# Performance work log

Measured on AMD Instinct MI355X. Metric: run time of the kernel, lower is better.

## Reference

```python
import jax, jax.numpy as jnp
import numpy as np

N = 100000      # nodes
E = 1600000     # edges
IN, H, OUT = 128, 128, 64
FUSION_W = 0.5


def setup_inputs() -> dict:
    key = jax.random.key(0)
    ks = jax.random.split(key, 10)
    x = jax.random.normal(ks[0], (N, IN), dtype=jnp.float32)
    edge_index = jax.random.randint(ks[1], (2, E), 0, N, dtype=jnp.int32)

    def lin(k, fi, fo):
        return jax.random.normal(k, (fi, fo), dtype=jnp.float32) / np.float32(np.sqrt(fi))

    return {
        "x": x,
        "edge_index": edge_index,
        "gnn_W1": lin(ks[2], IN, H),  "gnn_b1": jnp.zeros((H,), jnp.float32),
        "gnn_W2": lin(ks[3], H, OUT), "gnn_b2": jnp.zeros((OUT,), jnp.float32),
        "mlp_W1": lin(ks[4], IN, H),  "mlp_b1": jnp.zeros((H,), jnp.float32),
        "mlp_W2": lin(ks[5], H, OUT), "mlp_b2": jnp.zeros((OUT,), jnp.float32),
    }


def _gcn_conv(x, W, b, src, dst, deg_inv_sqrt, deg_inv):
    # GCNConv: x' = D^{-1/2} (A + I) D^{-1/2} (x W) + b, deg counts self-loops
    h = x @ W                                     # [N, F_out]
    norm = deg_inv_sqrt[src] * deg_inv_sqrt[dst]  # [E]
    agg = jax.ops.segment_sum(h[src] * norm[:, None], dst, num_segments=N)
    # self-loop contribution has norm 1/deg
    return agg + h * deg_inv[:, None] + b


def reference(x, edge_index, gnn_W1, gnn_b1, gnn_W2, gnn_b2,
              mlp_W1, mlp_b1, mlp_W2, mlp_b2):
    src, dst = edge_index[0], edge_index[1]
    # in-degree including self-loops (PyG GCNConv default add_self_loops=True)
    deg = 1.0 + jax.ops.segment_sum(jnp.ones((E,), jnp.float32), dst, num_segments=N)
    deg_inv_sqrt = jax.lax.rsqrt(deg)
    deg_inv = 1.0 / deg

    # GNN branch (dropout is identity in eval mode)
    h = jax.nn.relu(_gcn_conv(x, gnn_W1, gnn_b1, src, dst, deg_inv_sqrt, deg_inv))
    z_gnn = _gcn_conv(h, gnn_W2, gnn_b2, src, dst, deg_inv_sqrt, deg_inv)

    # MLP branch
    z_mlp = jax.nn.relu(x @ mlp_W1 + mlp_b1) @ mlp_W2 + mlp_b2

    return FUSION_W * z_gnn + (1.0 - FUSION_W) * z_mlp
```

## Files before the change

kernel.cpp:

```cpp
#include <hip/hip_runtime.h>
#include <hip/hip_fp16.h>

static constexpr int IN_F = 128;
static constexpr int FCAP = 6144;

typedef _Float16 half8 __attribute__((ext_vector_type(8)));
typedef _Float16 half4 __attribute__((ext_vector_type(4)));
typedef float f32x4 __attribute__((ext_vector_type(4)));
typedef float f32x2 __attribute__((ext_vector_type(2)));

__device__ inline void acc_fp8x8(uint2 u, f32x2* a) {
    a[0] += __builtin_amdgcn_cvt_pk_f32_fp8(u.x, false);
    a[1] += __builtin_amdgcn_cvt_pk_f32_fp8(u.x, true);
    a[2] += __builtin_amdgcn_cvt_pk_f32_fp8(u.y, false);
    a[3] += __builtin_amdgcn_cvt_pk_f32_fp8(u.y, true);
}
__device__ inline void acc_fp8x4(unsigned u, f32x2* a) {
    a[0] += __builtin_amdgcn_cvt_pk_f32_fp8(u, false);
    a[1] += __builtin_amdgcn_cvt_pk_f32_fp8(u, true);
}
__device__ inline void fp8x8_to_f32(uint2 u, float* f) {
    f32x2 a0 = __builtin_amdgcn_cvt_pk_f32_fp8(u.x, false);
    f32x2 a1 = __builtin_amdgcn_cvt_pk_f32_fp8(u.x, true);
    f32x2 a2 = __builtin_amdgcn_cvt_pk_f32_fp8(u.y, false);
    f32x2 a3 = __builtin_amdgcn_cvt_pk_f32_fp8(u.y, true);
    f[0] = a0[0]; f[1] = a0[1]; f[2] = a1[0]; f[3] = a1[1];
    f[4] = a2[0]; f[5] = a2[1]; f[6] = a3[0]; f[7] = a3[1];
}
__device__ inline void fp8x4_to_f32(unsigned u, float* f) {
    f32x2 a0 = __builtin_amdgcn_cvt_pk_f32_fp8(u, false);
    f32x2 a1 = __builtin_amdgcn_cvt_pk_f32_fp8(u, true);
    f[0] = a0[0]; f[1] = a0[1]; f[2] = a1[0]; f[3] = a1[1];
}
__device__ inline unsigned char f32_to_fp8(float v) {
    return (unsigned char)__builtin_amdgcn_cvt_pk_fp8_f32(v, v, 0, false);
}


__global__ __launch_bounds__(1024) void kb_count(const int* __restrict__ dst,
                                                 int* __restrict__ bcount, int E) {
    __shared__ int cnt[16][512];
    const int tid = threadIdx.x;
    const int wv  = tid >> 6;
    for (int i = tid; i < 16 * 512; i += 1024) (&cnt[0][0])[i] = 0;
    __syncthreads();
#pragma unroll
    for (int q = 0; q < 8; ++q) {
        int i = blockIdx.x * 8192 + q * 1024 + tid;
        if (i < E) atomicAdd(&cnt[wv][dst[i] >> 8], 1);
    }
    __syncthreads();
    if (tid < 512) {
        int run = 0;
#pragma unroll
        for (int w = 0; w < 16; ++w) run += cnt[w][tid];
        if (run > 0) atomicAdd(&bcount[tid], run);
    }
}

__global__ __launch_bounds__(512) void k_scanb(const int* __restrict__ bcount,
                                               int* __restrict__ bbase,
                                               int* __restrict__ bcursor, int NB) {
    __shared__ int s[512];
    const int tid = threadIdx.x;
    int v = (tid < NB) ? bcount[tid] : 0;
    s[tid] = v;
    __syncthreads();
    int inc = v;
#pragma unroll
    for (int off = 1; off < 512; off <<= 1) {
        int add = (tid >= off) ? s[tid - off] : 0;
        __syncthreads();
        s[tid] = inc = inc + add;
        __syncthreads();
    }
    if (tid < NB) { bbase[tid] = inc - v; bcursor[tid] = inc - v; }
    if (tid == NB - 1) bbase[NB] = inc;
}

__global__ __launch_bounds__(1024) void kb_move(const int* __restrict__ src,
                                                const int* __restrict__ dst,
                                                int* __restrict__ bcursor,
                                                unsigned* __restrict__ recs, int E) {
    __shared__ int cnt[16][512];
    __shared__ int gbase[512];
    const int tid = threadIdx.x;
    const int wv  = tid >> 6;
    for (int i = tid; i < 16 * 512; i += 1024) (&cnt[0][0])[i] = 0;
    __syncthreads();

    int bq[8];
    unsigned rq[8];
#pragma unroll
    for (int q = 0; q < 8; ++q) {
        int i = blockIdx.x * 8192 + q * 1024 + tid;
        if (i < E) {
            int d = dst[i];
            int s = src[i];
            bq[q] = d >> 8;
            rq[q] = (unsigned)(((d & 255) << 17) | s);
            atomicAdd(&cnt[wv][bq[q]], 1);
        } else {
            bq[q] = -1;
            rq[q] = 0u;
        }
    }
    __syncthreads();
    if (tid < 512) {
        int run = 0;
#pragma unroll
        for (int w = 0; w < 16; ++w) {
            int t = cnt[w][tid];
            cnt[w][tid] = run;
            run += t;
        }
        gbase[tid] = (run > 0) ? atomicAdd(&bcursor[tid], run) : 0;
    }
    __syncthreads();
#pragma unroll
    for (int q = 0; q < 8; ++q) {
        if (bq[q] >= 0) {
            int p = gbase[bq[q]] + atomicAdd(&cnt[wv][bq[q]], 1);
            recs[p] = rq[q];
        }
    }
}

__global__ __launch_bounds__(512) void kb_fill_lds(const unsigned* __restrict__ recs,
                                                   const int* __restrict__ bbase,
                                                   int* __restrict__ row_ptr,
                                                   float* __restrict__ dis,
                                                   int* __restrict__ csr, int n) {
    __shared__ int hist[256];
    __shared__ int sc[256];
    __shared__ int base[257];
    __shared__ int cur[256];
    __shared__ int stage[FCAP];
    const int tid   = threadIdx.x;
    const int b     = blockIdx.x;
    const int s     = bbase[b], e = bbase[b + 1];
    const int nbase = b << 8;

    if (tid < 256) hist[tid] = 0;
    __syncthreads();
    for (int i = s + tid; i < e; i += 512)
        atomicAdd(&hist[recs[i] >> 17], 1);
    __syncthreads();

    const int v = (tid < 256) ? hist[tid] : 0;
    if (tid < 256) sc[tid] = v;
    __syncthreads();
    int inc = v;
#pragma unroll
    for (int off = 1; off < 256; off <<= 1) {
        int add = (tid >= off && tid < 256) ? sc[tid - off] : 0;
        __syncthreads();
        if (tid < 256) sc[tid] = inc = inc + add;
        __syncthreads();
    }
    if (tid < 256) {
        const int excl = inc - v;
        base[tid] = excl;
        if (tid == 255) base[256] = inc;
        cur[tid] = 0;

        const int idx = nbase + tid;
        if (idx < n) {
            row_ptr[idx] = s + excl;
            dis[idx] = rsqrtf(1.0f + (float)v);
        }
        if (idx == n) row_ptr[n] = s + excl;
        if (tid == 255 && nbase + 256 == n) row_ptr[n] = s + inc;
    }
    __syncthreads();

    for (int i = s + tid; i < e; i += 512) {
        unsigned r = recs[i];
        int dl = (int)(r >> 17);
        int slot = base[dl] + atomicAdd(&cur[dl], 1);
        int sr = (int)(r & 0x1FFFFu);
        if (slot < FCAP) stage[slot] = sr;
        else csr[s + slot] = sr;
    }
    __syncthreads();

    const int total = e - s;
    const int lim = total < FCAP ? total : FCAP;
    for (int i = tid; i < lim; i += 512)
        csr[s + i] = stage[i];
}

__global__ __launch_bounds__(256) void k_prep_w(const float* __restrict__ gW1,
                                                const float* __restrict__ mW1,
                                                const float* __restrict__ mW2,
                                                const float* __restrict__ gW2,
                                                _Float16* __restrict__ tg1,
                                                _Float16* __restrict__ tm1,
                                                _Float16* __restrict__ tm2,
                                                _Float16* __restrict__ tg2) {
    int i = blockIdx.x * 256 + threadIdx.x;
    if (i < 16384)      { int j = i;         int f = j >> 7, k = j & 127; tg1[j] = (_Float16)gW1[k * 128 + f]; }
    else if (i < 32768) { int j = i - 16384; int f = j >> 7, k = j & 127; tm1[j] = (_Float16)mW1[k * 128 + f]; }
    else if (i < 40960) { int j = i - 32768; int f = j >> 7, k = j & 127; tm2[j] = (_Float16)mW2[k * 64 + f]; }
    else if (i < 49152) { int j = i - 40960; int f = j >> 7, k = j & 127; tg2[j] = (_Float16)gW2[k * 64 + f]; }
}

__global__ __launch_bounds__(256) void k_dual_mfma(const float* __restrict__ x,
                                                   const _Float16* __restrict__ tg1,
                                                   const _Float16* __restrict__ tm1,
                                                   const _Float16* __restrict__ tm2,
                                                   const float* __restrict__ b1,
                                                   const float* __restrict__ b2,
                                                   const float* __restrict__ dis,
                                                   unsigned char* __restrict__ h1,
                                                   _Float16* __restrict__ z, int nrows) {
    __shared__ _Float16 As[64 * 128];
    __shared__ _Float16 Ws[128 * 128];
    _Float16* Ms = As;
    const int tid  = threadIdx.x;
    const int row0 = blockIdx.x * 64;

#pragma unroll
    for (int p = 0; p < 4; ++p) {
        int sid = p * 256 + tid;
        int r = sid >> 4, s = sid & 15;
        int gr = row0 + r;
        uint4 v = make_uint4(0, 0, 0, 0);
        if (gr < nrows) {
            const float4 f0 = *reinterpret_cast<const float4*>(x + (size_t)gr * 128 + s * 8);
            const float4 f1 = *reinterpret_cast<const float4*>(x + (size_t)gr * 128 + s * 8 + 4);
            _Float16 t[8] = {(_Float16)f0.x, (_Float16)f0.y, (_Float16)f0.z, (_Float16)f0.w,
                             (_Float16)f1.x, (_Float16)f1.y, (_Float16)f1.z, (_Float16)f1.w};
            v = *reinterpret_cast<uint4*>(t);
        }
        *reinterpret_cast<uint4*>(&As[r * 128 + ((s ^ (r & 7)) * 8)]) = v;
    }
#pragma unroll
    for (int p = 0; p < 8; ++p) {
        int sid = p * 256 + tid;
        int r = sid >> 4, s = sid & 15;
        uint4 v = *reinterpret_cast<const uint4*>(tg1 + (size_t)r * 128 + s * 8);
        *reinterpret_cast<uint4*>(&Ws[r * 128 + ((s ^ (r & 7)) * 8)]) = v;
    }
    __syncthreads();

    const int lane = tid & 63;
    const int wv   = tid >> 6;
    const int mrow = wv * 16 + (lane & 15);
    const int kg   = lane >> 4;
    const int grow = row0 + wv * 16 + kg * 4;

    half8 a[4];
#pragma unroll
    for (int kk = 0; kk < 4; ++kk)
        a[kk] = *reinterpret_cast<const half8*>(&As[mrow * 128 + (((kk * 4 + kg) ^ (mrow & 7)) * 8)]);

    float dvals[4];
#pragma unroll
    for (int j = 0; j < 4; ++j)
        dvals[j] = (grow + j < nrows) ? dis[grow + j] : 0.f;

#pragma unroll
    for (int ct = 0; ct < 8; ++ct) {
        const int ncol = ct * 16 + (lane & 15);
        f32x4 acc = {0.f, 0.f, 0.f, 0.f};
#pragma unroll
        for (int kk = 0; kk < 4; ++kk) {
            half8 b = *reinterpret_cast<const half8*>(&Ws[ncol * 128 + (((kk * 4 + kg) ^ (ncol & 7)) * 8)]);
            acc = __builtin_amdgcn_mfma_f32_16x16x32_f16(a[kk], b, acc, 0, 0, 0);
        }
#pragma unroll
        for (int j = 0; j < 4; ++j)
            if (grow + j < nrows)
                h1[(size_t)(grow + j) * 128 + ncol] = f32_to_fp8(acc[j] * dvals[j]);
    }
    __syncthreads();

#pragma unroll
    for (int p = 0; p < 8; ++p) {
        int sid = p * 256 + tid;
        int r = sid >> 4, s = sid & 15;
        uint4 v = *reinterpret_cast<const uint4*>(tm1 + (size_t)r * 128 + s * 8);
        *reinterpret_cast<uint4*>(&Ws[r * 128 + ((s ^ (r & 7)) * 8)]) = v;
    }
    __syncthreads();

#pragma unroll
    for (int ct = 0; ct < 8; ++ct) {
        const int ncol = ct * 16 + (lane & 15);
        f32x4 acc = {0.f, 0.f, 0.f, 0.f};
#pragma unroll
        for (int kk = 0; kk < 4; ++kk) {
            half8 b = *reinterpret_cast<const half8*>(&Ws[ncol * 128 + (((kk * 4 + kg) ^ (ncol & 7)) * 8)]);
            acc = __builtin_amdgcn_mfma_f32_16x16x32_f16(a[kk], b, acc, 0, 0, 0);
        }
        const float bias = b1[ncol];
#pragma unroll
        for (int j = 0; j < 4; ++j) {
            int r = wv * 16 + kg * 4 + j;
            float v = fmaxf((float)acc[j] + bias, 0.f);
            Ms[r * 128 + (((ncol >> 3) ^ (r & 7)) * 8) + (ncol & 7)] = (_Float16)v;
        }
    }
    __syncthreads();

#pragma unroll
    for (int p = 0; p < 4; ++p) {
        int sid = p * 256 + tid;
        int r = sid >> 4, s = sid & 15;
        uint4 v = *reinterpret_cast<const uint4*>(tm2 + (size_t)r * 128 + s * 8);
        *reinterpret_cast<uint4*>(&Ws[r * 128 + ((s ^ (r & 7)) * 8)]) = v;
    }
    __syncthreads();

    half8 am[4];
#pragma unroll
    for (int kk = 0; kk < 4; ++kk)
        am[kk] = *reinterpret_cast<const half8*>(&Ms[mrow * 128 + (((kk * 4 + kg) ^ (mrow & 7)) * 8)]);

#pragma unroll
    for (int ct = 0; ct < 4; ++ct) {
        const int ncol = ct * 16 + (lane & 15);
        f32x4 acc = {0.f, 0.f, 0.f, 0.f};
#pragma unroll
        for (int kk = 0; kk < 4; ++kk) {
            half8 b = *reinterpret_cast<const half8*>(&Ws[ncol * 128 + (((kk * 4 + kg) ^ (ncol & 7)) * 8)]);
            acc = __builtin_amdgcn_mfma_f32_16x16x32_f16(am[kk], b, acc, 0, 0, 0);
        }
        const float bias = b2[ncol];
#pragma unroll
        for (int j = 0; j < 4; ++j)
            if (grow + j < nrows)
                z[(size_t)(grow + j) * 64 + ncol] = (_Float16)((float)acc[j] + bias);
    }
}

__global__ __launch_bounds__(256) void k_mm64(const _Float16* __restrict__ A,
                                              const _Float16* __restrict__ Wt,
                                              const float* __restrict__ dis,
                                              unsigned char* __restrict__ C, int nrows) {
    __shared__ _Float16 As[64 * 128];
    __shared__ _Float16 Ws[64 * 128];
    const int tid  = threadIdx.x;
    const int row0 = blockIdx.x * 64;

#pragma unroll
    for (int p = 0; p < 4; ++p) {
        int sid = p * 256 + tid;
        int r = sid >> 4, s = sid & 15;
        int gr = row0 + r;
        uint4 v = make_uint4(0, 0, 0, 0);
        if (gr < nrows) v = *reinterpret_cast<const uint4*>(A + (size_t)gr * 128 + s * 8);
        *reinterpret_cast<uint4*>(&As[r * 128 + ((s ^ (r & 7)) * 8)]) = v;
    }
#pragma unroll
    for (int p = 0; p < 4; ++p) {
        int sid = p * 256 + tid;
        int r = sid >> 4, s = sid & 15;
        uint4 v = *reinterpret_cast<const uint4*>(Wt + (size_t)r * 128 + s * 8);
        *reinterpret_cast<uint4*>(&Ws[r * 128 + ((s ^ (r & 7)) * 8)]) = v;
    }
    __syncthreads();

    const int lane = tid & 63;
    const int wv   = tid >> 6;
    const int mrow = wv * 16 + (lane & 15);
    const int kg   = lane >> 4;
    const int grow = row0 + wv * 16 + kg * 4;

    half8 a[4];
#pragma unroll
    for (int kk = 0; kk < 4; ++kk)
        a[kk] = *reinterpret_cast<const half8*>(&As[mrow * 128 + (((kk * 4 + kg) ^ (mrow & 7)) * 8)]);

    float dvals[4];
#pragma unroll
    for (int j = 0; j < 4; ++j)
        dvals[j] = (grow + j < nrows) ? dis[grow + j] : 0.f;

#pragma unroll
    for (int ct = 0; ct < 4; ++ct) {
        const int ncol = ct * 16 + (lane & 15);
        f32x4 acc = {0.f, 0.f, 0.f, 0.f};
#pragma unroll
        for (int kk = 0; kk < 4; ++kk) {
            half8 b = *reinterpret_cast<const half8*>(&Ws[ncol * 128 + (((kk * 4 + kg) ^ (ncol & 7)) * 8)]);
            acc = __builtin_amdgcn_mfma_f32_16x16x32_f16(a[kk], b, acc, 0, 0, 0);
        }
#pragma unroll
        for (int j = 0; j < 4; ++j)
            if (grow + j < nrows)
                C[(size_t)(grow + j) * 64 + ncol] = f32_to_fp8(acc[j] * dvals[j]);
    }
}

__global__ __launch_bounds__(256) void k_agg1(const int* __restrict__ rp,
                                              const int* __restrict__ csr,
                                              const float* __restrict__ dis,
                                              const unsigned char* __restrict__ h1,
                                              const float* __restrict__ b,
                                              _Float16* __restrict__ out, int n) {
    const int tid  = threadIdx.x;
    const int node = blockIdx.x * 4 + (tid >> 6);
    if (node >= n) return;
    const int lane = tid & 63;
    const int g    = lane >> 4;
    const int c0   = (lane & 15) * 8;
    const int start = rp[node], end = rp[node + 1];

    f32x2 acc[4] = {{0.f, 0.f}, {0.f, 0.f}, {0.f, 0.f}, {0.f, 0.f}};

    int j = start + g;
    for (; j + 12 < end; j += 16) {
        int s0 = csr[j];
        int s1 = csr[j + 4];
        int s2 = csr[j + 8];
        int s3 = csr[j + 12];
        uint2 u0 = *reinterpret_cast<const uint2*>(h1 + (size_t)s0 * 128 + c0);
        uint2 u1 = *reinterpret_cast<const uint2*>(h1 + (size_t)s1 * 128 + c0);
        uint2 u2 = *reinterpret_cast<const uint2*>(h1 + (size_t)s2 * 128 + c0);
        uint2 u3 = *reinterpret_cast<const uint2*>(h1 + (size_t)s3 * 128 + c0);
        acc_fp8x8(u0, acc);
        acc_fp8x8(u1, acc);
        acc_fp8x8(u2, acc);
        acc_fp8x8(u3, acc);
    }
    for (; j < end; j += 4) {
        int s0 = csr[j];
        uint2 u0 = *reinterpret_cast<const uint2*>(h1 + (size_t)s0 * 128 + c0);
        acc_fp8x8(u0, acc);
    }

    float av[8] = {acc[0][0], acc[0][1], acc[1][0], acc[1][1],
                   acc[2][0], acc[2][1], acc[3][0], acc[3][1]};
#pragma unroll
    for (int k = 0; k < 8; ++k) {
        av[k] += __shfl_xor(av[k], 16);
        av[k] += __shfl_xor(av[k], 32);
    }

    if (g == 0) {
        const float dd = dis[node];
        uint2 un = *reinterpret_cast<const uint2*>(h1 + (size_t)node * 128 + c0);
        float fn[8];
        fp8x8_to_f32(un, fn);
        const float4 bv0 = *reinterpret_cast<const float4*>(b + c0);
        const float4 bv1 = *reinterpret_cast<const float4*>(b + c0 + 4);
        const float bb[8] = {bv0.x, bv0.y, bv0.z, bv0.w, bv1.x, bv1.y, bv1.z, bv1.w};
        half8 o;
#pragma unroll
        for (int k = 0; k < 8; ++k)
            o[k] = (_Float16)fmaxf(dd * (av[k] + fn[k]) + bb[k], 0.f);
        *reinterpret_cast<half8*>(out + (size_t)node * 128 + c0) = o;
    }
}

__global__ __launch_bounds__(256) void k_agg2(const int* __restrict__ rp,
                                              const int* __restrict__ csr,
                                              const float* __restrict__ dis,
                                              const unsigned char* __restrict__ h2,
                                              const float* __restrict__ b,
                                              const _Float16* __restrict__ zmlp,
                                              float* __restrict__ out, int n) {
    const int tid  = threadIdx.x;
    const int node = blockIdx.x * 4 + (tid >> 6);
    if (node >= n) return;
    const int lane = tid & 63;
    const int g    = lane >> 4;
    const int c0   = (lane & 15) * 4;
    const int start = rp[node], end = rp[node + 1];

    f32x2 acc[2] = {{0.f, 0.f}, {0.f, 0.f}};

    int j = start + g;
    for (; j + 12 < end; j += 16) {
        int s0 = csr[j];
        int s1 = csr[j + 4];
        int s2 = csr[j + 8];
        int s3 = csr[j + 12];
        unsigned u0 = *reinterpret_cast<const unsigned*>(h2 + (size_t)s0 * 64 + c0);
        unsigned u1 = *reinterpret_cast<const unsigned*>(h2 + (size_t)s1 * 64 + c0);
        unsigned u2 = *reinterpret_cast<const unsigned*>(h2 + (size_t)s2 * 64 + c0);
        unsigned u3 = *reinterpret_cast<const unsigned*>(h2 + (size_t)s3 * 64 + c0);
        acc_fp8x4(u0, acc);
        acc_fp8x4(u1, acc);
        acc_fp8x4(u2, acc);
        acc_fp8x4(u3, acc);
    }
    for (; j < end; j += 4) {
        int s0 = csr[j];
        unsigned u0 = *reinterpret_cast<const unsigned*>(h2 + (size_t)s0 * 64 + c0);
        acc_fp8x4(u0, acc);
    }

    float av[4] = {acc[0][0], acc[0][1], acc[1][0], acc[1][1]};
#pragma unroll
    for (int k = 0; k < 4; ++k) {
        av[k] += __shfl_xor(av[k], 16);
        av[k] += __shfl_xor(av[k], 32);
    }

    if (g == 0) {
        const float dd = dis[node];
        unsigned un = *reinterpret_cast<const unsigned*>(h2 + (size_t)node * 64 + c0);
        float fn[4];
        fp8x4_to_f32(un, fn);
        half4 zm = *reinterpret_cast<const half4*>(zmlp + (size_t)node * 64 + c0);
        const float4 bv = *reinterpret_cast<const float4*>(b + c0);
        const float bb[4] = {bv.x, bv.y, bv.z, bv.w};
        float4 o;
        float* op = &o.x;
#pragma unroll
        for (int k = 0; k < 4; ++k)
            op[k] = 0.5f * ((dd * (av[k] + fn[k]) + bb[k]) + (float)zm[k]);
        *reinterpret_cast<float4*>(out + (size_t)node * 64 + c0) = o;
    }
}

extern "C" void kernel_launch(void* const* d_in, const int* in_sizes, int n_in,
                              void* d_out, int out_size, void* d_ws, size_t ws_size,
                              hipStream_t stream) {
    const float* x      = (const float*)d_in[0];
    const int* edge_idx = (const int*)d_in[1];
    const float* gnn_W1 = (const float*)d_in[2];
    const float* gnn_b1 = (const float*)d_in[3];
    const float* gnn_W2 = (const float*)d_in[4];
    const float* gnn_b2 = (const float*)d_in[5];
    const float* mlp_W1 = (const float*)d_in[6];
    const float* mlp_b1 = (const float*)d_in[7];
    const float* mlp_W2 = (const float*)d_in[8];
    const float* mlp_b2 = (const float*)d_in[9];
    float* out = (float*)d_out;

    const int N = in_sizes[0] / IN_F;
    const int E = in_sizes[1] / 2;
    const int* src = edge_idx;
    const int* dst = edge_idx + E;

    const int NB = (N + 255) >> 8;

    char* wp = (char*)d_ws;
    int* row_ptr   = (int*)wp;            wp += ((size_t)N + 4) * sizeof(int);
    int* bbase     = (int*)wp;            wp += 516 * sizeof(int);
    int* bcursor   = (int*)wp;            wp += 512 * sizeof(int);
    int* bcount    = (int*)wp;            wp += 512 * sizeof(int);
    int* csr       = (int*)wp;            wp += (size_t)E * sizeof(int);
    unsigned* recs = (unsigned*)wp;       wp += (size_t)E * sizeof(unsigned);
    float* dis     = (float*)wp;          wp += (size_t)N * sizeof(float);
    _Float16* tg1  = (_Float16*)wp;       wp += 16384 * sizeof(_Float16);
    _Float16* tm1  = (_Float16*)wp;       wp += 16384 * sizeof(_Float16);
    _Float16* tm2  = (_Float16*)wp;       wp += 8192 * sizeof(_Float16);
    _Float16* tg2  = (_Float16*)wp;       wp += 8192 * sizeof(_Float16);
    unsigned char* h1 = (unsigned char*)wp;  wp += (size_t)N * 128;
    _Float16* hmid = (_Float16*)wp;       wp += (size_t)N * 128 * sizeof(_Float16);
    unsigned char* h2 = (unsigned char*)wp;  wp += (size_t)N * 64;
    wp = (char*)(((uintptr_t)wp + 15) & ~(uintptr_t)15);
    _Float16* zmlp = (_Float16*)wp;       wp += (size_t)N * 64 * sizeof(_Float16);

    k_prep_w<<<192, 256, 0, stream>>>(gnn_W1, mlp_W1, mlp_W2, gnn_W2, tg1, tm1, tm2, tg2);

    hipMemsetAsync(bcount, 0, 512 * sizeof(int), stream);
    const int mvblocks = (E + 8191) / 8192;
    kb_count<<<mvblocks, 1024, 0, stream>>>(dst, bcount, E);
    k_scanb<<<1, 512, 0, stream>>>(bcount, bbase, bcursor, NB);
    kb_move<<<mvblocks, 1024, 0, stream>>>(src, dst, bcursor, recs, E);
    kb_fill_lds<<<NB, 512, 0, stream>>>(recs, bbase, row_ptr, dis, csr, N);

    const int gblocks = (N + 63) / 64;

    k_dual_mfma<<<gblocks, 256, 0, stream>>>(x, tg1, tm1, tm2, mlp_b1, mlp_b2, dis, h1, zmlp, N);

    k_agg1<<<(N + 3) / 4, 256, 0, stream>>>(row_ptr, csr, dis, h1, gnn_b1, hmid, N);

    k_mm64<<<gblocks, 256, 0, stream>>>(hmid, tg2, dis, h2, N);

    k_agg2<<<(N + 3) / 4, 256, 0, stream>>>(row_ptr, csr, dis, h2, gnn_b2, zmlp, out, N);
}
```

Baseline: 204.9 us.

## Split GCN aggregations into two feature-half passes for cache locality

```diff
diff --git a/kernel.cpp b/kernel.cpp
--- a/kernel.cpp
+++ b/kernel.cpp
@@ -338,7 +338,9 @@
 __global__ __launch_bounds__(256) void k_mm64(const _Float16* __restrict__ A,
                                               const _Float16* __restrict__ Wt,
                                               const float* __restrict__ dis,
-                                              unsigned char* __restrict__ C, int nrows) {
+                                              unsigned char* __restrict__ Ca,
+                                              unsigned char* __restrict__ Cb,
+                                              int nrows) {
     __shared__ _Float16 As[64 * 128];
     __shared__ _Float16 Ws[64 * 128];
     const int tid  = threadIdx.x;
@@ -387,45 +389,41 @@
             half8 b = *reinterpret_cast<const half8*>(&Ws[ncol * 128 + (((kk * 4 + kg) ^ (ncol & 7)) * 8)]);
             acc = __builtin_amdgcn_mfma_f32_16x16x32_f16(a[kk], b, acc, 0, 0, 0);
         }
+        unsigned char* base = (ncol < 32) ? Ca : Cb;
+        const int colh = ncol & 31;
 #pragma unroll
         for (int j = 0; j < 4; ++j)
             if (grow + j < nrows)
-                C[(size_t)(grow + j) * 64 + ncol] = f32_to_fp8(acc[j] * dvals[j]);
-    }
-}
-
-__global__ __launch_bounds__(256) void k_agg1(const int* __restrict__ rp,
-                                              const int* __restrict__ csr,
-                                              const float* __restrict__ dis,
-                                              const unsigned char* __restrict__ h1,
-                                              const float* __restrict__ b,
-                                              _Float16* __restrict__ out, int n) {
+                base[(size_t)(grow + j) * 32 + colh] = f32_to_fp8(acc[j] * dvals[j]);
+    }
+}
+
+__global__ __launch_bounds__(256) void k_agg1h(const int* __restrict__ rp,
+                                               const int* __restrict__ csr,
+                                               const float* __restrict__ dis,
+                                               const unsigned char* __restrict__ h1,
+                                               const float* __restrict__ b,
+                                               _Float16* __restrict__ out, int n, int h0) {
     const int tid  = threadIdx.x;
     const int node = blockIdx.x * 4 + (tid >> 6);
     if (node >= n) return;
     const int lane = tid & 63;
-    const int g    = lane >> 4;
-    const int c0   = (lane & 15) * 8;
+    const int g    = lane >> 3;
+    const int c0   = h0 + (lane & 7) * 8;
     const int start = rp[node], end = rp[node + 1];
 
     f32x2 acc[4] = {{0.f, 0.f}, {0.f, 0.f}, {0.f, 0.f}, {0.f, 0.f}};
 
     int j = start + g;
-    for (; j + 12 < end; j += 16) {
+    for (; j + 8 < end; j += 16) {
         int s0 = csr[j];
-        int s1 = csr[j + 4];
-        int s2 = csr[j + 8];
-        int s3 = csr[j + 12];
+        int s1 = csr[j + 8];
         uint2 u0 = *reinterpret_cast<const uint2*>(h1 + (size_t)s0 * 128 + c0);
         uint2 u1 = *reinterpret_cast<const uint2*>(h1 + (size_t)s1 * 128 + c0);
-        uint2 u2 = *reinterpret_cast<const uint2*>(h1 + (size_t)s2 * 128 + c0);
-        uint2 u3 = *reinterpret_cast<const uint2*>(h1 + (size_t)s3 * 128 + c0);
         acc_fp8x8(u0, acc);
         acc_fp8x8(u1, acc);
-        acc_fp8x8(u2, acc);
-        acc_fp8x8(u3, acc);
-    }
-    for (; j < end; j += 4) {
+    }
+    if (j < end) {
         int s0 = csr[j];
         uint2 u0 = *reinterpret_cast<const uint2*>(h1 + (size_t)s0 * 128 + c0);
         acc_fp8x8(u0, acc);
@@ -435,6 +433,7 @@
                    acc[2][0], acc[2][1], acc[3][0], acc[3][1]};
 #pragma unroll
     for (int k = 0; k < 8; ++k) {
+        av[k] += __shfl_xor(av[k], 8);
         av[k] += __shfl_xor(av[k], 16);
         av[k] += __shfl_xor(av[k], 32);
     }
@@ -455,65 +454,60 @@
     }
 }
 
-__global__ __launch_bounds__(256) void k_agg2(const int* __restrict__ rp,
-                                              const int* __restrict__ csr,
-                                              const float* __restrict__ dis,
-                                              const unsigned char* __restrict__ h2,
-                                              const float* __restrict__ b,
-                                              const _Float16* __restrict__ zmlp,
-                                              float* __restrict__ out, int n) {
+__global__ __launch_bounds__(256) void k_agg2h(const int* __restrict__ rp,
+                                               const int* __restrict__ csr,
+                                               const float* __restrict__ dis,
+                                               const unsigned char* __restrict__ h2h,
+                                               const float* __restrict__ b,
+                                               const _Float16* __restrict__ zmlp,
+                                               float* __restrict__ out, int n, int h0) {
     const int tid  = threadIdx.x;
     const int node = blockIdx.x * 4 + (tid >> 6);
     if (node >= n) return;
     const int lane = tid & 63;
-    const int g    = lane >> 4;
-    const int c0   = (lane & 15) * 4;
+    const int g    = lane >> 3;
+    const int c0   = (lane & 7) * 4;
     const int start = rp[node], end = rp[node + 1];
 
     f32x2 acc[2] = {{0.f, 0.f}, {0.f, 0.f}};
 
     int j = start + g;
-    for (; j + 12 < end; j += 16) {
+    for (; j + 8 < end; j += 16) {
         int s0 = csr[j];
-        int s1 = csr[j + 4];
-        int s2 = csr[j + 8];
-        int s3 = csr[j + 12];
-        unsigned u0 = *reinterpret_cast<const unsigned*>(h2 + (size_t)s0 * 64 + c0);
-        unsigned u1 = *reinterpret_cast<const unsigned*>(h2 + (size_t)s1 * 64 + c0);
-        unsigned u2 = *reinterpret_cast<const unsigned*>(h2 + (size_t)s2 * 64 + c0);
-        unsigned u3 = *reinterpret_cast<const unsigned*>(h2 + (size_t)s3 * 64 + c0);
+        int s1 = csr[j + 8];
+        unsigned u0 = *reinterpret_cast<const unsigned*>(h2h + (size_t)s0 * 32 + c0);
+        unsigned u1 = *reinterpret_cast<const unsigned*>(h2h + (size_t)s1 * 32 + c0);
         acc_fp8x4(u0, acc);
         acc_fp8x4(u1, acc);
-        acc_fp8x4(u2, acc);
-        acc_fp8x4(u3, acc);
-    }
-    for (; j < end; j += 4) {
+    }
+    if (j < end) {
         int s0 = csr[j];
-        unsigned u0 = *reinterpret_cast<const unsigned*>(h2 + (size_t)s0 * 64 + c0);
+        unsigned u0 = *reinterpret_cast<const unsigned*>(h2h + (size_t)s0 * 32 + c0);
         acc_fp8x4(u0, acc);
     }
 
     float av[4] = {acc[0][0], acc[0][1], acc[1][0], acc[1][1]};
 #pragma unroll
     for (int k = 0; k < 4; ++k) {
+        av[k] += __shfl_xor(av[k], 8);
         av[k] += __shfl_xor(av[k], 16);
         av[k] += __shfl_xor(av[k], 32);
     }
 
     if (g == 0) {
         const float dd = dis[node];
-        unsigned un = *reinterpret_cast<const unsigned*>(h2 + (size_t)node * 64 + c0);
+        unsigned un = *reinterpret_cast<const unsigned*>(h2h + (size_t)node * 32 + c0);
         float fn[4];
         fp8x4_to_f32(un, fn);
-        half4 zm = *reinterpret_cast<const half4*>(zmlp + (size_t)node * 64 + c0);
-        const float4 bv = *reinterpret_cast<const float4*>(b + c0);
+        half4 zm = *reinterpret_cast<const half4*>(zmlp + (size_t)node * 64 + h0 + c0);
+        const float4 bv = *reinterpret_cast<const float4*>(b + h0 + c0);
         const float bb[4] = {bv.x, bv.y, bv.z, bv.w};
         float4 o;
         float* op = &o.x;
 #pragma unroll
         for (int k = 0; k < 4; ++k)
             op[k] = 0.5f * ((dd * (av[k] + fn[k]) + bb[k]) + (float)zm[k]);
-        *reinterpret_cast<float4*>(out + (size_t)node * 64 + c0) = o;
+        *reinterpret_cast<float4*>(out + (size_t)node * 64 + h0 + c0) = o;
     }
 }
 
@@ -553,7 +547,8 @@
     _Float16* tg2  = (_Float16*)wp;       wp += 8192 * sizeof(_Float16);
     unsigned char* h1 = (unsigned char*)wp;  wp += (size_t)N * 128;
     _Float16* hmid = (_Float16*)wp;       wp += (size_t)N * 128 * sizeof(_Float16);
-    unsigned char* h2 = (unsigned char*)wp;  wp += (size_t)N * 64;
+    unsigned char* h2a = (unsigned char*)wp; wp += (size_t)N * 32;
+    unsigned char* h2b = (unsigned char*)wp; wp += (size_t)N * 32;
     wp = (char*)(((uintptr_t)wp + 15) & ~(uintptr_t)15);
     _Float16* zmlp = (_Float16*)wp;       wp += (size_t)N * 64 * sizeof(_Float16);
 
@@ -567,12 +562,15 @@
     kb_fill_lds<<<NB, 512, 0, stream>>>(recs, bbase, row_ptr, dis, csr, N);
 
     const int gblocks = (N + 63) / 64;
+    const int ablocks = (N + 3) / 4;
 
     k_dual_mfma<<<gblocks, 256, 0, stream>>>(x, tg1, tm1, tm2, mlp_b1, mlp_b2, dis, h1, zmlp, N);
 
-    k_agg1<<<(N + 3) / 4, 256, 0, stream>>>(row_ptr, csr, dis, h1, gnn_b1, hmid, N);
-
-    k_mm64<<<gblocks, 256, 0, stream>>>(hmid, tg2, dis, h2, N);
-
-    k_agg2<<<(N + 3) / 4, 256, 0, stream>>>(row_ptr, csr, dis, h2, gnn_b2, zmlp, out, N);
-}
+    k_agg1h<<<ablocks, 256, 0, stream>>>(row_ptr, csr, dis, h1, gnn_b1, hmid, N, 0);
+    k_agg1h<<<ablocks, 256, 0, stream>>>(row_ptr, csr, dis, h1, gnn_b1, hmid, N, 64);
+
+    k_mm64<<<gblocks, 256, 0, stream>>>(hmid, tg2, dis, h2a, h2b, N);
+
+    k_agg2h<<<ablocks, 256, 0, stream>>>(row_ptr, csr, dis, h2a, gnn_b2, zmlp, out, N, 0);
+    k_agg2h<<<ablocks, 256, 0, stream>>>(row_ptr, csr, dis, h2b, gnn_b2, zmlp, out, N, 32);
+}
```

Measured after the change: 263.9 us. 1.29x slower.
